# Kernel tuning notes

Measured on AMD Instinct MI355X. Metric: run time of the kernel, lower is better.

Reference implementation:

```python
import jax, jax.numpy as jnp
import numpy as np
from jax import lax

BN_EPS = 1e-5


def _conv(x, w, b, stride):
    # x: [N,C,H,W], w: [O,I,3,3], stride 2, padding 1
    y = lax.conv_general_dilated(
        x, w, window_strides=(stride, stride), padding=((1, 1), (1, 1)),
        dimension_numbers=('NCHW', 'OIHW', 'NCHW'))
    return y + b[None, :, None, None]


def _batchnorm(x, gamma, beta):
    # training-mode BN: batch statistics over (N,H,W)
    mean = jnp.mean(x, axis=(0, 2, 3), keepdims=True)
    var = jnp.var(x, axis=(0, 2, 3), keepdims=True)
    xn = (x - mean) * lax.rsqrt(var + BN_EPS)
    return xn * gamma[None, :, None, None] + beta[None, :, None, None]


def _maxpool2(x):
    return lax.reduce_window(x, -jnp.inf, lax.max, (1, 1, 2, 2), (1, 1, 2, 2), 'VALID')


def setup_inputs() -> dict:
    key = jax.random.key(0)
    ks = jax.random.split(key, 8)
    B, C, H, W = 128, 3, 224, 224
    x = jax.random.normal(ks[0], (B, C, H, W), dtype=jnp.float32)
    conv1_w = jax.random.normal(ks[1], (16, 3, 3, 3), dtype=jnp.float32) * (1.0 / np.sqrt(3 * 9))
    conv1_b = jnp.zeros((16,), dtype=jnp.float32)
    bn1_g = jnp.ones((16,), dtype=jnp.float32)
    bn1_b = jnp.zeros((16,), dtype=jnp.float32)
    conv2_w = jax.random.normal(ks[2], (32, 16, 3, 3), dtype=jnp.float32) * (1.0 / np.sqrt(16 * 9))
    conv2_b = jnp.zeros((32,), dtype=jnp.float32)
    bn2_g = jnp.ones((32,), dtype=jnp.float32)
    bn2_b = jnp.zeros((32,), dtype=jnp.float32)
    fc_w = jax.random.normal(ks[3], (1, 32), dtype=jnp.float32) * (1.0 / np.sqrt(32))
    fc_b = jnp.zeros((1,), dtype=jnp.float32)
    return dict(x=x, conv1_w=conv1_w, conv1_b=conv1_b, bn1_g=bn1_g, bn1_b=bn1_b,
                conv2_w=conv2_w, conv2_b=conv2_b, bn2_g=bn2_g, bn2_b=bn2_b,
                fc_w=fc_w, fc_b=fc_b)


def reference(x, conv1_w, conv1_b, bn1_g, bn1_b, conv2_w, conv2_b, bn2_g, bn2_b, fc_w, fc_b):
    h = jax.nn.relu(_batchnorm(_conv(x, conv1_w, conv1_b, 2), bn1_g, bn1_b))   # [B,16,112,112]
    h = _maxpool2(h)                                                           # [B,16,56,56]
    h = jax.nn.relu(_batchnorm(_conv(h, conv2_w, conv2_b, 2), bn2_g, bn2_b))   # [B,32,28,28]
    h = jnp.mean(h, axis=(2, 3))                                               # AdaptiveAvgPool2d((1,1)) -> [B,32]
    logits = h @ fc_w.T + fc_b                                                 # [B,1]
    # Quantum circuit: RY(theta) on all wires, CNOT chain, <Z_0>.
    # Z on the control wire commutes with every CNOT -> expval = cos(theta).
    probs = jnp.cos(logits)                                                    # [B,1]
    return jnp.concatenate((probs, 1.0 - probs), axis=-1)                      # [B,2]
```

## Files before the change

### kernel.cpp

```cpp
#include <hip/hip_runtime.h>
#include <math.h>

#define BATCH 128
#define CIN 3
#define H 224
#define W 224
#define C1 16
#define HP 56
#define WP 56
#define C2 32
#define H2 28
#define W2 28

__global__ __launch_bounds__(256) void conv1_fused_k(
    const float* __restrict__ x, const float* __restrict__ w1,
    const float* __restrict__ b1, float2* __restrict__ mm,
    float* __restrict__ s_sum, float* __restrict__ s_sq)
{
    __shared__ float red[4][8], redq[4][8];
    const int tid = threadIdx.x;
    const int t = blockIdx.x * 256 + tid;
    const int c0 = blockIdx.y * 8;
    const int n = t / 1568;
    const int r = t % 1568;
    const int phh = r / 56;
    const int pw  = r % 56;
    const int rbase = 8 * phh - 1;
    const int cbase = 4 * pw;
    const bool topok = phh > 0;
    const bool pwok  = pw > 0;

    float accA[8][4], accB[8][4];
#pragma unroll
    for (int j = 0; j < 8; ++j) {
        const float bb = b1[c0 + j];
#pragma unroll
        for (int q = 0; q < 4; ++q) { accA[j][q] = bb; accB[j][q] = bb; }
    }

#pragma unroll
    for (int ci = 0; ci < CIN; ++ci) {
        const float* img = x + (n * CIN + ci) * (H * W);
        float p[9][5];
#pragma unroll
        for (int l = 0; l < 9; ++l) {
            const int ih = max(rbase + l, 0);
            const float* rowp = img + ih * W;
            const float4 f4 = *(const float4*)(rowp + cbase);
            const float lf = rowp[max(cbase - 1, 0)];
            const bool rok = (l > 0) || topok;
            p[l][0] = (rok && pwok) ? lf : 0.0f;
            p[l][1] = rok ? f4.x : 0.0f;
            p[l][2] = rok ? f4.y : 0.0f;
            p[l][3] = rok ? f4.z : 0.0f;
            p[l][4] = rok ? f4.w : 0.0f;
        }
#pragma unroll
        for (int j = 0; j < 8; ++j) {
            const float* wc = w1 + ((c0 + j) * CIN + ci) * 9;
#pragma unroll
            for (int kh = 0; kh < 3; ++kh) {
#pragma unroll
                for (int kw = 0; kw < 3; ++kw) {
                    const float wv = wc[kh * 3 + kw];
                    accA[j][0] += wv * p[kh][kw];
                    accA[j][1] += wv * p[kh][kw + 2];
                    accA[j][2] += wv * p[kh + 2][kw];
                    accA[j][3] += wv * p[kh + 2][kw + 2];
                    accB[j][0] += wv * p[4 + kh][kw];
                    accB[j][1] += wv * p[4 + kh][kw + 2];
                    accB[j][2] += wv * p[6 + kh][kw];
                    accB[j][3] += wv * p[6 + kh][kw + 2];
                }
            }
        }
    }

#pragma unroll
    for (int j = 0; j < 8; ++j) {
        const int o = (n * C1 + c0 + j) * (HP * WP) + (2 * phh) * WP + pw;
        const float a0 = accA[j][0], a1 = accA[j][1], a2 = accA[j][2], a3 = accA[j][3];
        const float b0 = accB[j][0], b1v = accB[j][1], b2v = accB[j][2], b3 = accB[j][3];
        mm[o] = make_float2(fmaxf(fmaxf(a0, a1), fmaxf(a2, a3)),
                            fminf(fminf(a0, a1), fminf(a2, a3)));
        mm[o + WP] = make_float2(fmaxf(fmaxf(b0, b1v), fmaxf(b2v, b3)),
                                 fminf(fminf(b0, b1v), fminf(b2v, b3)));
        float s = a0 + a1 + a2 + a3 + b0 + b1v + b2v + b3;
        float q = a0 * a0 + a1 * a1 + a2 * a2 + a3 * a3
                + b0 * b0 + b1v * b1v + b2v * b2v + b3 * b3;
#pragma unroll
        for (int off = 32; off > 0; off >>= 1) {
            s += __shfl_xor(s, off);
            q += __shfl_xor(q, off);
        }
        if ((tid & 63) == 0) { red[tid >> 6][j] = s; redq[tid >> 6][j] = q; }
    }
    __syncthreads();
    if (tid < 8) {
        atomicAdd(&s_sum[c0 + tid],
                  red[0][tid] + red[1][tid] + red[2][tid] + red[3][tid]);
    } else if (tid < 16) {
        const int j = tid - 8;
        atomicAdd(&s_sq[c0 + j],
                  redq[0][j] + redq[1][j] + redq[2][j] + redq[3][j]);
    }
}

__global__ __launch_bounds__(256) void conv2_k(
    const float2* __restrict__ mm,
    const float* __restrict__ s1sum, const float* __restrict__ s1sq,
    const float* __restrict__ g1, const float* __restrict__ be1,
    const float* __restrict__ w2, const float* __restrict__ b2,
    float* __restrict__ y2,
    float* __restrict__ s_sum, float* __restrict__ s_sq)
{
    __shared__ float red[4][8], redq[4][8];
    const int tid = threadIdx.x;
    const int t = blockIdx.x * 256 + tid;
    const int c0 = blockIdx.y * 8;
    const int n = t / 784;
    const int p = t % 784;
    const int oh = p / W2, ow = p % W2;
    const bool topok = oh > 0;
    const bool owok  = ow > 0;
    const float inv1 = 1.0f / (float)(BATCH * 112 * 112);

    float acc[8];
#pragma unroll
    for (int c = 0; c < 8; ++c) acc[c] = b2[c0 + c];

#pragma unroll 2
    for (int ci = 0; ci < C1; ++ci) {
        const float mean = s1sum[ci] * inv1;
        const float var  = s1sq[ci] * inv1 - mean * mean;
        const float s1 = g1[ci] * rsqrtf(var + 1e-5f);
        const float t1 = be1[ci] - mean * s1;

        const float2* pl = mm + (n * C1 + ci) * (HP * WP);
        float v[3][3];
#pragma unroll
        for (int kh = 0; kh < 3; ++kh) {
            const int ih = max(2 * oh - 1 + kh, 0);
            const float2* rowp = pl + ih * WP;
            const float4 f4 = *(const float4*)(rowp + 2 * ow);
            const float2 lp = rowp[max(2 * ow - 1, 0)];
            const bool rok = (kh > 0) || topok;
            const float h0 = fmaxf(0.0f, fmaxf(s1 * lp.x + t1, s1 * lp.y + t1));
            const float h1 = fmaxf(0.0f, fmaxf(s1 * f4.x + t1, s1 * f4.y + t1));
            const float h2 = fmaxf(0.0f, fmaxf(s1 * f4.z + t1, s1 * f4.w + t1));
            v[kh][0] = (rok && owok) ? h0 : 0.0f;
            v[kh][1] = rok ? h1 : 0.0f;
            v[kh][2] = rok ? h2 : 0.0f;
        }
#pragma unroll
        for (int c = 0; c < 8; ++c) {
            const float* wc = w2 + ((c0 + c) * C1 + ci) * 9;
            float a = acc[c];
            a += wc[0] * v[0][0]; a += wc[1] * v[0][1]; a += wc[2] * v[0][2];
            a += wc[3] * v[1][0]; a += wc[4] * v[1][1]; a += wc[5] * v[1][2];
            a += wc[6] * v[2][0]; a += wc[7] * v[2][1]; a += wc[8] * v[2][2];
            acc[c] = a;
        }
    }

#pragma unroll
    for (int c = 0; c < 8; ++c) {
        const float a = acc[c];
        y2[(n * C2 + c0 + c) * (H2 * W2) + p] = a;
        float s = a, q = a * a;
#pragma unroll
        for (int off = 32; off > 0; off >>= 1) {
            s += __shfl_xor(s, off);
            q += __shfl_xor(q, off);
        }
        if ((tid & 63) == 0) { red[tid >> 6][c] = s; redq[tid >> 6][c] = q; }
    }
    __syncthreads();
    if (tid < 8) {
        atomicAdd(&s_sum[c0 + tid],
                  red[0][tid] + red[1][tid] + red[2][tid] + red[3][tid]);
    } else if (tid < 16) {
        const int c = tid - 8;
        atomicAdd(&s_sq[c0 + c],
                  redq[0][c] + redq[1][c] + redq[2][c] + redq[3][c]);
    }
}

__global__ __launch_bounds__(256) void head_fused_k(
    const float* __restrict__ y2,
    const float* __restrict__ s2sum, const float* __restrict__ s2sq,
    const float* __restrict__ g2, const float* __restrict__ be2,
    const float* __restrict__ fcw, const float* __restrict__ fcb,
    float* __restrict__ out)
{
    __shared__ float feat[C2];
    const int n = blockIdx.x;
    const int tid = threadIdx.x;
    const int wave = tid >> 6, lane = tid & 63;
    const float inv2 = 1.0f / (float)(BATCH * H2 * W2);
#pragma unroll
    for (int k = 0; k < 8; ++k) {
        const int c = wave * 8 + k;
        const float mean = s2sum[c] * inv2;
        const float var  = s2sq[c] * inv2 - mean * mean;
        const float s = g2[c] * rsqrtf(var + 1e-5f);
        const float t = be2[c] - mean * s;
        const float4* yp = (const float4*)(y2 + (n * C2 + c) * (H2 * W2));
        float a = 0.0f;
        for (int i = lane; i < 196; i += 64) {
            const float4 v = yp[i];
            a += fmaxf(0.0f, s * v.x + t) + fmaxf(0.0f, s * v.y + t)
               + fmaxf(0.0f, s * v.z + t) + fmaxf(0.0f, s * v.w + t);
        }
#pragma unroll
        for (int off = 32; off > 0; off >>= 1) a += __shfl_xor(a, off);
        if (lane == 0) feat[c] = a * (1.0f / (H2 * W2));
    }
    __syncthreads();
    if (tid == 0) {
        float logit = fcb[0];
#pragma unroll
        for (int c = 0; c < C2; ++c) logit += feat[c] * fcw[c];
        const float pc = cosf(logit);
        out[2 * n]     = pc;
        out[2 * n + 1] = 1.0f - pc;
    }
}

extern "C" void kernel_launch(void* const* d_in, const int* in_sizes, int n_in,
                              void* d_out, int out_size, void* d_ws, size_t ws_size,
                              hipStream_t stream) {
    const float* x   = (const float*)d_in[0];
    const float* w1  = (const float*)d_in[1];
    const float* b1  = (const float*)d_in[2];
    const float* g1  = (const float*)d_in[3];
    const float* be1 = (const float*)d_in[4];
    const float* w2  = (const float*)d_in[5];
    const float* b2  = (const float*)d_in[6];
    const float* g2  = (const float*)d_in[7];
    const float* be2 = (const float*)d_in[8];
    const float* fcw = (const float*)d_in[9];
    const float* fcb = (const float*)d_in[10];
    float* out = (float*)d_out;

    float* ws = (float*)d_ws;
    float2* mm = (float2*)ws;
    float* y2 = ws + (size_t)2 * BATCH * C1 * HP * WP;
    float* stats = y2 + (size_t)BATCH * C2 * H2 * W2;
    float* s1sum = stats;
    float* s1sq  = stats + 16;
    float* s2sum = stats + 32;
    float* s2sq  = stats + 64;

    hipMemsetAsync(stats, 0, 96 * sizeof(float), stream);

    conv1_fused_k<<<dim3(784, 2), 256, 0, stream>>>(x, w1, b1, mm, s1sum, s1sq);
    conv2_k<<<dim3(392, 4), 256, 0, stream>>>(mm, s1sum, s1sq, g1, be1,
                                              w2, b2, y2, s2sum, s2sq);
    head_fused_k<<<BATCH, 256, 0, stream>>>(y2, s2sum, s2sq, g2, be2,
                                            fcw, fcb, out);
}
```

Measured before the change: 215.0 us.

## Halve conv1 per-thread work to one pooled output and raise occupancy

Each thread of conv1_fused_k now computes one pooled 2x2 window instead of two vertically stacked ones. It streams each of the 5 input rows straight into the accumulators rather than buffering 9 rows in a register array. The grid doubles in x and launch bounds ask for 8 blocks per CU, cutting register pressure so more waves can hide load latency. In exchange, overlapping input rows are loaded twice as often across threads and the block-level atomics for BN statistics double.

```diff
diff --git a/kernel.cpp b/kernel.cpp
--- a/kernel.cpp
+++ b/kernel.cpp
@@ -12,7 +12,7 @@
 #define H2 28
 #define W2 28
 
-__global__ __launch_bounds__(256) void conv1_fused_k(
+__global__ __launch_bounds__(256, 8) void conv1_fused_k(
     const float* __restrict__ x, const float* __restrict__ w1,
     const float* __restrict__ b1, float2* __restrict__ mm,
     float* __restrict__ s_sum, float* __restrict__ s_sq)
@@ -21,56 +21,55 @@
     const int tid = threadIdx.x;
     const int t = blockIdx.x * 256 + tid;
     const int c0 = blockIdx.y * 8;
-    const int n = t / 1568;
-    const int r = t % 1568;
-    const int phh = r / 56;
-    const int pw  = r % 56;
-    const int rbase = 8 * phh - 1;
+    const int n = t / 3136;
+    const int r = t % 3136;
+    const int ph = r / 56;
+    const int pw = r % 56;
+    const int rbase = 4 * ph - 1;
     const int cbase = 4 * pw;
-    const bool topok = phh > 0;
+    const bool topok = ph > 0;
     const bool pwok  = pw > 0;
 
-    float accA[8][4], accB[8][4];
+    float acc[8][4];
 #pragma unroll
     for (int j = 0; j < 8; ++j) {
         const float bb = b1[c0 + j];
 #pragma unroll
-        for (int q = 0; q < 4; ++q) { accA[j][q] = bb; accB[j][q] = bb; }
+        for (int q = 0; q < 4; ++q) acc[j][q] = bb;
     }
 
 #pragma unroll
     for (int ci = 0; ci < CIN; ++ci) {
         const float* img = x + (n * CIN + ci) * (H * W);
-        float p[9][5];
-#pragma unroll
-        for (int l = 0; l < 9; ++l) {
+#pragma unroll
+        for (int l = 0; l < 5; ++l) {
             const int ih = max(rbase + l, 0);
             const float* rowp = img + ih * W;
             const float4 f4 = *(const float4*)(rowp + cbase);
             const float lf = rowp[max(cbase - 1, 0)];
             const bool rok = (l > 0) || topok;
-            p[l][0] = (rok && pwok) ? lf : 0.0f;
-            p[l][1] = rok ? f4.x : 0.0f;
-            p[l][2] = rok ? f4.y : 0.0f;
-            p[l][3] = rok ? f4.z : 0.0f;
-            p[l][4] = rok ? f4.w : 0.0f;
-        }
-#pragma unroll
-        for (int j = 0; j < 8; ++j) {
-            const float* wc = w1 + ((c0 + j) * CIN + ci) * 9;
-#pragma unroll
-            for (int kh = 0; kh < 3; ++kh) {
-#pragma unroll
-                for (int kw = 0; kw < 3; ++kw) {
-                    const float wv = wc[kh * 3 + kw];
-                    accA[j][0] += wv * p[kh][kw];
-                    accA[j][1] += wv * p[kh][kw + 2];
-                    accA[j][2] += wv * p[kh + 2][kw];
-                    accA[j][3] += wv * p[kh + 2][kw + 2];
-                    accB[j][0] += wv * p[4 + kh][kw];
-                    accB[j][1] += wv * p[4 + kh][kw + 2];
-                    accB[j][2] += wv * p[6 + kh][kw];
-                    accB[j][3] += wv * p[6 + kh][kw + 2];
+            const float p0 = (rok && pwok) ? lf : 0.0f;
+            const float p1 = rok ? f4.x : 0.0f;
+            const float p2 = rok ? f4.y : 0.0f;
+            const float p3 = rok ? f4.z : 0.0f;
+            const float p4 = rok ? f4.w : 0.0f;
+#pragma unroll
+            for (int j = 0; j < 8; ++j) {
+                const float* wc = w1 + ((c0 + j) * CIN + ci) * 9;
+                if (l < 3) {
+                    const float wa = wc[l * 3 + 0];
+                    const float wb = wc[l * 3 + 1];
+                    const float wd = wc[l * 3 + 2];
+                    acc[j][0] += wa * p0 + wb * p1 + wd * p2;
+                    acc[j][1] += wa * p2 + wb * p3 + wd * p4;
+                }
+                if (l >= 2) {
+                    const int kh = l - 2;
+                    const float wa = wc[kh * 3 + 0];
+                    const float wb = wc[kh * 3 + 1];
+                    const float wd = wc[kh * 3 + 2];
+                    acc[j][2] += wa * p0 + wb * p1 + wd * p2;
+                    acc[j][3] += wa * p2 + wb * p3 + wd * p4;
                 }
             }
         }
@@ -78,16 +77,12 @@
 
 #pragma unroll
     for (int j = 0; j < 8; ++j) {
-        const int o = (n * C1 + c0 + j) * (HP * WP) + (2 * phh) * WP + pw;
-        const float a0 = accA[j][0], a1 = accA[j][1], a2 = accA[j][2], a3 = accA[j][3];
-        const float b0 = accB[j][0], b1v = accB[j][1], b2v = accB[j][2], b3 = accB[j][3];
+        const int o = (n * C1 + c0 + j) * (HP * WP) + ph * WP + pw;
+        const float a0 = acc[j][0], a1 = acc[j][1], a2 = acc[j][2], a3 = acc[j][3];
         mm[o] = make_float2(fmaxf(fmaxf(a0, a1), fmaxf(a2, a3)),
                             fminf(fminf(a0, a1), fminf(a2, a3)));
-        mm[o + WP] = make_float2(fmaxf(fmaxf(b0, b1v), fmaxf(b2v, b3)),
-                                 fminf(fminf(b0, b1v), fminf(b2v, b3)));
-        float s = a0 + a1 + a2 + a3 + b0 + b1v + b2v + b3;
-        float q = a0 * a0 + a1 * a1 + a2 * a2 + a3 * a3
-                + b0 * b0 + b1v * b1v + b2v * b2v + b3 * b3;
+        float s = a0 + a1 + a2 + a3;
+        float q = a0 * a0 + a1 * a1 + a2 * a2 + a3 * a3;
 #pragma unroll
         for (int off = 32; off > 0; off >>= 1) {
             s += __shfl_xor(s, off);
@@ -254,7 +249,7 @@
 
     hipMemsetAsync(stats, 0, 96 * sizeof(float), stream);
 
-    conv1_fused_k<<<dim3(784, 2), 256, 0, stream>>>(x, w1, b1, mm, s1sum, s1sq);
+    conv1_fused_k<<<dim3(1568, 2), 256, 0, stream>>>(x, w1, b1, mm, s1sum, s1sq);
     conv2_k<<<dim3(392, 4), 256, 0, stream>>>(mm, s1sum, s1sq, g1, be1,
                                               w2, b2, y2, s2sum, s2sq);
     head_fused_k<<<BATCH, 256, 0, stream>>>(y2, s2sum, s2sq, g2, be2,
```

Result: slower. 359.7 us (+67.3%).
